# Performance work log

Hardware: AMD Instinct MI355X
Metric: run time of the kernel (lower is better)

Reference implementation:

```python
import jax, jax.numpy as jnp
import numpy as np

G = 512          # graphs per batch
NPG = 90         # nodes per graph (AAL-90 atlas)
N = G * NPG      # 46080 total nodes
DEG = 20
E = N * DEG      # 921600 edges
F_IN = 90
H = 64           # hidden_channels (args.hc)
K = 70           # sort-pool k


def setup_inputs() -> dict:
    key = jax.random.key(0)
    ks = jax.random.split(key, 14)
    x = jax.random.normal(ks[0], (N, F_IN), dtype=jnp.float32)
    # edges kept within each graph (realistic PyG batching)
    gid = jax.random.randint(ks[1], (E,), 0, G)
    src = gid * NPG + jax.random.randint(ks[2], (E,), 0, NPG)
    dst = gid * NPG + jax.random.randint(ks[3], (E,), 0, NPG)
    edge_index = jnp.stack([src, dst]).astype(jnp.int64)
    batch = (jnp.arange(N) // NPG).astype(jnp.int64)
    s_in = 1.0 / np.sqrt(F_IN)
    s_h = 1.0 / np.sqrt(H)
    s_p = 1.0 / np.sqrt(H * K)
    # SAGEConv: out = mean_aggr(x_j) @ W_l + x_i @ W_r + b
    W1l = jax.random.uniform(ks[4], (F_IN, H), jnp.float32, -s_in, s_in)
    W1r = jax.random.uniform(ks[5], (F_IN, H), jnp.float32, -s_in, s_in)
    b1 = jnp.zeros((H,), jnp.float32)
    W2l = jax.random.uniform(ks[6], (H, H), jnp.float32, -s_h, s_h)
    W2r = jax.random.uniform(ks[7], (H, H), jnp.float32, -s_h, s_h)
    b2 = jnp.zeros((H,), jnp.float32)
    Wl1 = jax.random.uniform(ks[8], (H * K, H), jnp.float32, -s_p, s_p)
    bl1 = jax.random.uniform(ks[9], (H,), jnp.float32, -s_p, s_p)
    Wl2 = jax.random.uniform(ks[10], (H, 1), jnp.float32, -s_h, s_h)
    bl2 = jax.random.uniform(ks[11], (1,), jnp.float32, -s_h, s_h)
    return {"x": x, "edge_index": edge_index, "batch": batch,
            "W1l": W1l, "W1r": W1r, "b1": b1,
            "W2l": W2l, "W2r": W2r, "b2": b2,
            "Wl1": Wl1, "bl1": bl1, "Wl2": Wl2, "bl2": bl2}


def sage_conv(x, src, dst, Wl, Wr, b):
    # gather source features, scatter-mean to destinations
    msg = x[src]                                              # [E, F]
    s = jax.ops.segment_sum(msg, dst, num_segments=N)         # [N, F]
    cnt = jax.ops.segment_sum(jnp.ones((src.shape[0], 1), x.dtype),
                              dst, num_segments=N)            # [N, 1]
    mean = s / jnp.maximum(cnt, 1.0)
    return mean @ Wl + x @ Wr + b


def global_sort_pool(x, k):
    # nodes per graph are contiguous and fixed (NPG >= k, no padding needed)
    xr = x.reshape(G, NPG, H)
    order = jnp.argsort(-xr[:, :, -1], axis=1)[:, :k]          # sort by last channel, desc
    top = jnp.take_along_axis(xr, order[:, :, None], axis=1)   # [G, k, H]
    return top.reshape(G, k * H)


def reference(x, edge_index, batch, W1l, W1r, b1, W2l, W2r, b2, Wl1, bl1, Wl2, bl2):
    src, dst = edge_index[0], edge_index[1]
    h = sage_conv(x, src, dst, W1l, W1r, b1)       # conv1
    x_train = h
    h = jax.nn.relu(h)
    h = sage_conv(h, src, dst, W2l, W2r, b2)       # conv2
    p = global_sort_pool(h, K)                     # [G, K*H]
    # dropout is identity at eval time
    p = p @ Wl1 + bl1
    p = p @ Wl2 + bl2
    out = jnp.squeeze(jax.nn.sigmoid(p))           # [G]
    return out, x_train
```

## Files before the change

### kernel.cpp

```cpp
#include <hip/hip_runtime.h>

typedef unsigned short u16;
typedef unsigned int u32;
typedef unsigned char u8;
typedef unsigned long long u64;

#define GG   512
#define NPG  90
#define NTOT (GG*NPG)
#define NED  921600
#define FIN  90
#define HC   64
#define KP   70

#define SAD  90
#define SP   68
#define SR   67
#define SXW  46

#define WF_W1L 0
#define WF_W1R 5760
#define WF_W2L 11520
#define WF_W2R 15616
#define WF_B1  19712
#define WF_B2  19776
#define WF_FOLD 19840
#define WF_ZC  24320
#define WF_FLAG 24321

__device__ __forceinline__ float bf2f(u16 u) {
    union { u32 i; float f; } v; v.i = ((u32)u) << 16; return v.f;
}
__device__ __forceinline__ float bflo(u32 u) {
    union { u32 i; float f; } v; v.i = u << 16; return v.f;
}
__device__ __forceinline__ float bfhi(u32 u) {
    union { u32 i; float f; } v; v.i = u & 0xFFFF0000u; return v.f;
}
__device__ __forceinline__ u16 f2bf(float f) {
    union { float f; u32 i; } v; v.f = f;
    u32 r = (v.i + 0x7FFFu + ((v.i >> 16) & 1u)) >> 16;
    return (u16)r;
}
__device__ __forceinline__ float ldadp(const void* p, long long i, int isf32) {
    return isf32 ? ((const float*)p)[i] : bf2f(((const u16*)p)[i]);
}

__global__ __launch_bounds__(256) void k_pre(
    const u32* __restrict__ xw, const int* __restrict__ ei,
    const void* W1l, const void* W1r, const void* b1,
    const void* W2l, const void* W2r, const void* b2,
    const void* Wl1, const void* bl1, const void* Wl2, const void* bl2,
    float* __restrict__ A, float* __restrict__ wf)
{
    __shared__ int sf;
    const int t = threadIdx.x;
    const int b = blockIdx.x;

    if (b < 900) {
        int lane = t & 63;
        u32 v = (lane < 16) ? (u32)ei[lane] : 0u;
        u64 bb = __ballot((lane & 1) && (v != 0));
        bool wide = (bb == 0ull);
        int e0 = b * 1024 + t * 4;
        int s[4], d[4];
        if (wide) {
            uint4 s01 = *(const uint4*)(ei + 2 * e0);
            uint4 s23 = *(const uint4*)(ei + 2 * e0 + 4);
            uint4 d01 = *(const uint4*)(ei + 2 * (NED + e0));
            uint4 d23 = *(const uint4*)(ei + 2 * (NED + e0) + 4);
            s[0] = (int)s01.x; s[1] = (int)s01.z; s[2] = (int)s23.x; s[3] = (int)s23.z;
            d[0] = (int)d01.x; d[1] = (int)d01.z; d[2] = (int)d23.x; d[3] = (int)d23.z;
        } else {
            uint4 ss = *(const uint4*)(ei + e0);
            uint4 dd = *(const uint4*)(ei + NED + e0);
            s[0] = (int)ss.x; s[1] = (int)ss.y; s[2] = (int)ss.z; s[3] = (int)ss.w;
            d[0] = (int)dd.x; d[1] = (int)dd.y; d[2] = (int)dd.z; d[3] = (int)dd.w;
        }
        #pragma unroll
        for (int k = 0; k < 4; ++k) {
            int dk = d[k];
            if ((unsigned)dk >= NTOT) continue;
            int g = (unsigned)dk / NPG;
            int dl = dk - g * NPG;
            int ls = s[k] - g * NPG;
            if ((unsigned)ls >= NPG) continue;
            atomicAdd(&A[(size_t)g * 8100 + dl * NPG + ls], 1.0f);
        }
        return;
    }

    if (t < 64) {
        u32 e = (xw[t] >> 7) & 0xFF;
        u64 bb = __ballot(e >= 136);
        if (t == 0) sf = (bb != 0ull) ? 1 : 0;
    }
    __syncthreads();
    const int f32 = sf;

    if (b < 978) {
        int i = (b - 900) * 256 + t;
        if      (i < 5760)  wf[i] = ldadp(W1l, i, f32);
        else if (i < 11520) wf[i] = ldadp(W1r, i - 5760, f32);
        else if (i < 15616) wf[i] = ldadp(W2l, i - 11520, f32);
        else if (i < 19712) wf[i] = ldadp(W2r, i - 15616, f32);
        else if (i < 19776) wf[i] = ldadp(b1, i - 19712, f32);
        else if (i < 19840) wf[i] = ldadp(b2, i - 19776, f32);
        if (b == 900 && t == 0) wf[WF_FLAG] = f32 ? 1.0f : 0.0f;
    } else {
        int m = (b - 978) * 256 + t;
        if (m < 4480) {
            float s = 0.f;
            for (int j = 0; j < HC; ++j)
                s += ldadp(Wl1, (long long)m * HC + j, f32) * ldadp(Wl2, j, f32);
            wf[WF_FOLD + m] = s;
        } else if (m == 4480) {
            float s = ldadp(bl2, 0, f32);
            for (int j = 0; j < HC; ++j)
                s += ldadp(bl1, j, f32) * ldadp(Wl2, j, f32);
            wf[WF_ZC] = s;
        }
    }
}

__global__ __launch_bounds__(256, 2) void k_fused(
    const void* __restrict__ x, const float* __restrict__ A,
    const float* __restrict__ wf, void* __restrict__ dout)
{
    __shared__ __align__(16) char smem[57840];
    float* R1   = (float*)smem;
    float* As   = (float*)(smem + 24480);
    float* s_rc = (float*)(smem + 56880);
    float* s_key= (float*)(smem + 57264);
    float* s_red= (float*)(smem + 57648);
    u16*  s_ord = (u16*)(smem + 57680);

    const int g = blockIdx.x;
    const int t = threadIdx.x;
    const bool isf32 = (wf[WF_FLAG] > 0.5f);
    const float* Ag = A + (size_t)g * 8100;
    const float* xg32 = (const float*)x + (size_t)g * 8100;

    for (int p = t; p < 8100; p += 256) As[p] = Ag[p];
    if (!isf32) {
        const u32* src = (const u32*)((const u16*)x + (size_t)g * 8100);
        u32* sxw = (u32*)R1;
        for (int p = t; p < 4050; p += 256) {
            int row = p / 45, c = p - row * 45;
            sxw[row * SXW + c] = src[p];
        }
    }
    __syncthreads();
    if (t < NPG) {
        float s = 0.f;
        for (int k = 0; k < NPG; ++k) s += As[t * SAD + k];
        s_rc[t] = 1.0f / fmaxf(s, 1.0f);
    }

    const int trio = t & 31, jg = t >> 5, jb = jg * 8;
    const int n0 = trio * 3;
    int rows[3];
    #pragma unroll
    for (int i = 0; i < 3; ++i) rows[i] = (n0 + i < NPG) ? n0 + i : 0;

    float accP[3][8], accQ[3][8];
    {
        float4 q0 = *(const float4*)(wf + WF_B1 + jb);
        float4 q1 = *(const float4*)(wf + WF_B1 + jb + 4);
        float bias[8] = {q0.x,q0.y,q0.z,q0.w,q1.x,q1.y,q1.z,q1.w};
        #pragma unroll
        for (int i = 0; i < 3; ++i)
            #pragma unroll
            for (int j = 0; j < 8; ++j) { accP[i][j] = 0.f; accQ[i][j] = bias[j]; }
    }
    {
        const u32* sxw = (const u32*)R1;
        for (int kk = 0; kk < 45; ++kk) {
            const int k0 = 2 * kk;
            const float* wl = wf + WF_W1L + k0 * HC + jb;
            const float* wr = wf + WF_W1R + k0 * HC + jb;
            float4 l00 = *(const float4*)(wl);
            float4 l01 = *(const float4*)(wl + 4);
            float4 l10 = *(const float4*)(wl + HC);
            float4 l11 = *(const float4*)(wl + HC + 4);
            float4 r00 = *(const float4*)(wr);
            float4 r01 = *(const float4*)(wr + 4);
            float4 r10 = *(const float4*)(wr + HC);
            float4 r11 = *(const float4*)(wr + HC + 4);
            float wl0[8] = {l00.x,l00.y,l00.z,l00.w,l01.x,l01.y,l01.z,l01.w};
            float wl1[8] = {l10.x,l10.y,l10.z,l10.w,l11.x,l11.y,l11.z,l11.w};
            float wr0[8] = {r00.x,r00.y,r00.z,r00.w,r01.x,r01.y,r01.z,r01.w};
            float wr1[8] = {r10.x,r10.y,r10.z,r10.w,r11.x,r11.y,r11.z,r11.w};
            float x0[3], x1[3];
            if (!isf32) {
                #pragma unroll
                for (int i = 0; i < 3; ++i) {
                    u32 xv = sxw[rows[i] * SXW + kk];
                    x0[i] = bflo(xv); x1[i] = bfhi(xv);
                }
            } else {
                #pragma unroll
                for (int i = 0; i < 3; ++i) {
                    x0[i] = xg32[rows[i] * FIN + k0];
                    x1[i] = xg32[rows[i] * FIN + k0 + 1];
                }
            }
            #pragma unroll
            for (int i = 0; i < 3; ++i)
                #pragma unroll
                for (int j = 0; j < 8; ++j) {
                    accP[i][j] += x0[i] * wl0[j] + x1[i] * wl1[j];
                    accQ[i][j] += x0[i] * wr0[j] + x1[i] * wr1[j];
                }
        }
    }
    __syncthreads();
    #pragma unroll
    for (int i = 0; i < 3; ++i) {
        int n = n0 + i;
        if (n < NPG) {
            *(float4*)(R1 + n * SP + jb) =
                make_float4(accP[i][0], accP[i][1], accP[i][2], accP[i][3]);
            *(float4*)(R1 + n * SP + jb + 4) =
                make_float4(accP[i][4], accP[i][5], accP[i][6], accP[i][7]);
        }
    }
    __syncthreads();

    float r1v[3][8];
    {
        float accA[3][8];
        #pragma unroll
        for (int i = 0; i < 3; ++i)
            #pragma unroll
            for (int j = 0; j < 8; ++j) accA[i][j] = 0.f;
        for (int k = 0; k < NPG; ++k) {
            float4 p0 = *(const float4*)(R1 + k * SP + jb);
            float4 p1 = *(const float4*)(R1 + k * SP + jb + 4);
            float pv[8] = {p0.x,p0.y,p0.z,p0.w,p1.x,p1.y,p1.z,p1.w};
            float av[3];
            #pragma unroll
            for (int i = 0; i < 3; ++i) av[i] = As[rows[i] * SAD + k];
            #pragma unroll
            for (int i = 0; i < 3; ++i)
                #pragma unroll
                for (int j = 0; j < 8; ++j) accA[i][j] += av[i] * pv[j];
        }
        #pragma unroll
        for (int i = 0; i < 3; ++i) {
            int n = n0 + i;
            if (n < NPG) {
                float rc = s_rc[n];
                float h[8];
                #pragma unroll
                for (int j = 0; j < 8; ++j) h[j] = fmaf(rc, accA[i][j], accQ[i][j]);
                size_t base = 512 + (size_t)(g * NPG + n) * HC + jb;
                if (isf32) {
                    *(float4*)((float*)dout + base) = make_float4(h[0],h[1],h[2],h[3]);
                    *(float4*)((float*)dout + base + 4) = make_float4(h[4],h[5],h[6],h[7]);
                } else {
                    uint4 pk;
                    pk.x = (u32)f2bf(h[0]) | ((u32)f2bf(h[1]) << 16);
                    pk.y = (u32)f2bf(h[2]) | ((u32)f2bf(h[3]) << 16);
                    pk.z = (u32)f2bf(h[4]) | ((u32)f2bf(h[5]) << 16);
                    pk.w = (u32)f2bf(h[6]) | ((u32)f2bf(h[7]) << 16);
                    *(uint4*)((u16*)dout + base) = pk;
                }
                #pragma unroll
                for (int j = 0; j < 8; ++j) r1v[i][j] = fmaxf(h[j], 0.f);
            }
        }
    }
    __syncthreads();
    #pragma unroll
    for (int i = 0; i < 3; ++i) {
        int n = n0 + i;
        if (n < NPG)
            #pragma unroll
            for (int j = 0; j < 8; ++j) R1[n * SR + jb + j] = r1v[i][j];
    }
    __syncthreads();

    {
        float4 q0 = *(const float4*)(wf + WF_B2 + jb);
        float4 q1 = *(const float4*)(wf + WF_B2 + jb + 4);
        float bias[8] = {q0.x,q0.y,q0.z,q0.w,q1.x,q1.y,q1.z,q1.w};
        #pragma unroll
        for (int i = 0; i < 3; ++i)
            #pragma unroll
            for (int j = 0; j < 8; ++j) { accP[i][j] = 0.f; accQ[i][j] = bias[j]; }
    }
    for (int k = 0; k < HC; ++k) {
        const float* wl = wf + WF_W2L + k * HC + jb;
        const float* wr = wf + WF_W2R + k * HC + jb;
        float4 l0 = *(const float4*)(wl);
        float4 l1 = *(const float4*)(wl + 4);
        float4 r0 = *(const float4*)(wr);
        float4 r1q = *(const float4*)(wr + 4);
        float wlv[8] = {l0.x,l0.y,l0.z,l0.w,l1.x,l1.y,l1.z,l1.w};
        float wrv[8] = {r0.x,r0.y,r0.z,r0.w,r1q.x,r1q.y,r1q.z,r1q.w};
        float rv[3];
        #pragma unroll
        for (int i = 0; i < 3; ++i) rv[i] = R1[rows[i] * SR + k];
        #pragma unroll
        for (int i = 0; i < 3; ++i)
            #pragma unroll
            for (int j = 0; j < 8; ++j) {
                accP[i][j] += rv[i] * wlv[j];
                accQ[i][j] += rv[i] * wrv[j];
            }
    }
    __syncthreads();
    #pragma unroll
    for (int i = 0; i < 3; ++i) {
        int n = n0 + i;
        if (n < NPG) {
            *(float4*)(R1 + n * SP + jb) =
                make_float4(accP[i][0], accP[i][1], accP[i][2], accP[i][3]);
            *(float4*)(R1 + n * SP + jb + 4) =
                make_float4(accP[i][4], accP[i][5], accP[i][6], accP[i][7]);
        }
    }
    __syncthreads();

    float h2v[3][8];
    {
        float accA[3][8];
        #pragma unroll
        for (int i = 0; i < 3; ++i)
            #pragma unroll
            for (int j = 0; j < 8; ++j) accA[i][j] = 0.f;
        for (int k = 0; k < NPG; ++k) {
            float4 p0 = *(const float4*)(R1 + k * SP + jb);
            float4 p1 = *(const float4*)(R1 + k * SP + jb + 4);
            float pv[8] = {p0.x,p0.y,p0.z,p0.w,p1.x,p1.y,p1.z,p1.w};
            float av[3];
            #pragma unroll
            for (int i = 0; i < 3; ++i) av[i] = As[rows[i] * SAD + k];
            #pragma unroll
            for (int i = 0; i < 3; ++i)
                #pragma unroll
                for (int j = 0; j < 8; ++j) accA[i][j] += av[i] * pv[j];
        }
        #pragma unroll
        for (int i = 0; i < 3; ++i) {
            int n = n0 + i;
            if (n < NPG) {
                float rc = s_rc[n];
                #pragma unroll
                for (int j = 0; j < 8; ++j)
                    h2v[i][j] = fmaf(rc, accA[i][j], accQ[i][j]);
                if (jg == 7) s_key[n] = h2v[i][7];
            }
        }
    }
    __syncthreads();
    #pragma unroll
    for (int i = 0; i < 3; ++i) {
        int n = n0 + i;
        if (n < NPG)
            #pragma unroll
            for (int j = 0; j < 8; ++j) R1[n * SR + jb + j] = h2v[i][j];
    }
    if (t < NPG) {
        float my = s_key[t];
        int r = 0;
        for (int m2 = 0; m2 < NPG; ++m2) {
            float km = s_key[m2];
            r += (km > my) || (km == my && m2 < t);
        }
        if (r < KP) s_ord[r] = (u16)t;
    }
    __syncthreads();

    float zp = 0.f;
    for (int p = t; p < KP * HC; p += 256) {
        int i = p >> 6, c = p & 63;
        int nn = s_ord[i];
        zp += R1[nn * SR + c] * wf[WF_FOLD + p];
    }
    #pragma unroll
    for (int off = 32; off > 0; off >>= 1) zp += __shfl_down(zp, off);
    if ((t & 63) == 0) s_red[t >> 6] = zp;
    __syncthreads();
    if (t == 0) {
        float z = s_red[0] + s_red[1] + s_red[2] + s_red[3] + wf[WF_ZC];
        float sg = 1.0f / (1.0f + expf(-z));
        if (isf32) ((float*)dout)[g] = sg;
        else       ((u16*)dout)[g]   = f2bf(sg);
    }
}

extern "C" void kernel_launch(void* const* d_in, const int* in_sizes, int n_in,
                              void* d_out, int out_size, void* d_ws, size_t ws_size,
                              hipStream_t stream) {
    const void* x   = d_in[0];
    const int*  ei  = (const int*)d_in[1];
    const void* W1l = d_in[3];
    const void* W1r = d_in[4];
    const void* b1  = d_in[5];
    const void* W2l = d_in[6];
    const void* W2r = d_in[7];
    const void* b2  = d_in[8];
    const void* Wl1 = d_in[9];
    const void* bl1 = d_in[10];
    const void* Wl2 = d_in[11];
    const void* bl2 = d_in[12];

    char* ws   = (char*)d_ws;
    float* A   = (float*)(ws + 64);
    float* wf  = (float*)(ws + 64 + 16588800);

    hipMemsetAsync(A, 0, (size_t)GG * 8100 * sizeof(float), stream);
    k_pre<<<996, 256, 0, stream>>>((const u32*)x, ei, W1l, W1r, b1, W2l, W2r, b2,
                                   Wl1, bl1, Wl2, bl2, A, wf);
    k_fused<<<GG, 256, 0, stream>>>(x, A, wf, d_out);
}
```

Measured before the change: 222.9 us.

## Double fused-kernel block to 512 threads with 4 channels per thread and padded LDS

The fused per-graph kernel now uses 512 threads per block, each owning 3 nodes × 4 channels instead of 3 × 8, which halves per-thread register accumulators and raises wave count per graph. The adjacency and bf16 x tiles in LDS get row padding (91 and 47) to reduce bank conflicts on the strided column reads. The final reduction sums 8 wave partials. This adds more redundant weight and LDS loads per FMA, and with only 512 blocks it may still leave CUs underfilled.

```diff
diff --git a/kernel.cpp b/kernel.cpp
--- a/kernel.cpp
+++ b/kernel.cpp
@@ -13,10 +13,10 @@
 #define HC   64
 #define KP   70
 
-#define SAD  90
+#define SAD  91
 #define SP   68
 #define SR   67
-#define SXW  46
+#define SXW  47
 
 #define WF_W1L 0
 #define WF_W1R 5760
@@ -123,17 +123,17 @@
     }
 }
 
-__global__ __launch_bounds__(256, 2) void k_fused(
+__global__ __launch_bounds__(512, 4) void k_fused(
     const void* __restrict__ x, const float* __restrict__ A,
     const float* __restrict__ wf, void* __restrict__ dout)
 {
-    __shared__ __align__(16) char smem[57840];
+    __shared__ __align__(16) char smem[58176];
     float* R1   = (float*)smem;
     float* As   = (float*)(smem + 24480);
-    float* s_rc = (float*)(smem + 56880);
-    float* s_key= (float*)(smem + 57264);
-    float* s_red= (float*)(smem + 57648);
-    u16*  s_ord = (u16*)(smem + 57680);
+    float* s_rc = (float*)(smem + 57240);
+    float* s_key= (float*)(smem + 57600);
+    float* s_red= (float*)(smem + 57960);
+    u16*  s_ord = (u16*)(smem + 57992);
 
     const int g = blockIdx.x;
     const int t = threadIdx.x;
@@ -141,13 +141,22 @@
     const float* Ag = A + (size_t)g * 8100;
     const float* xg32 = (const float*)x + (size_t)g * 8100;
 
-    for (int p = t; p < 8100; p += 256) As[p] = Ag[p];
+    const int trio = t & 31, sl = t >> 5, jb = sl * 4;
+    const int n0 = trio * 3;
+    int rows[3];
+    #pragma unroll
+    for (int i = 0; i < 3; ++i) rows[i] = (n0 + i < NPG) ? n0 + i : 0;
+
+    for (int p = t; p < 8100; p += 512) {
+        int r = p / NPG, c = p - r * NPG;
+        As[r * SAD + c] = Ag[p];
+    }
     if (!isf32) {
         const u32* src = (const u32*)((const u16*)x + (size_t)g * 8100);
         u32* sxw = (u32*)R1;
-        for (int p = t; p < 4050; p += 256) {
-            int row = p / 45, c = p - row * 45;
-            sxw[row * SXW + c] = src[p];
+        for (int p = t; p < 4050; p += 512) {
+            int r = p / 45, c = p - r * 45;
+            sxw[r * SXW + c] = src[p];
         }
     }
     __syncthreads();
@@ -157,40 +166,27 @@
         s_rc[t] = 1.0f / fmaxf(s, 1.0f);
     }
 
-    const int trio = t & 31, jg = t >> 5, jb = jg * 8;
-    const int n0 = trio * 3;
-    int rows[3];
-    #pragma unroll
-    for (int i = 0; i < 3; ++i) rows[i] = (n0 + i < NPG) ? n0 + i : 0;
-
-    float accP[3][8], accQ[3][8];
-    {
-        float4 q0 = *(const float4*)(wf + WF_B1 + jb);
-        float4 q1 = *(const float4*)(wf + WF_B1 + jb + 4);
-        float bias[8] = {q0.x,q0.y,q0.z,q0.w,q1.x,q1.y,q1.z,q1.w};
+    float accP[3][4], accQ[3][4];
+    {
+        float4 bq = *(const float4*)(wf + WF_B1 + jb);
+        float bias[4] = {bq.x, bq.y, bq.z, bq.w};
         #pragma unroll
         for (int i = 0; i < 3; ++i)
             #pragma unroll
-            for (int j = 0; j < 8; ++j) { accP[i][j] = 0.f; accQ[i][j] = bias[j]; }
+            for (int j = 0; j < 4; ++j) { accP[i][j] = 0.f; accQ[i][j] = bias[j]; }
     }
     {
         const u32* sxw = (const u32*)R1;
         for (int kk = 0; kk < 45; ++kk) {
             const int k0 = 2 * kk;
-            const float* wl = wf + WF_W1L + k0 * HC + jb;
-            const float* wr = wf + WF_W1R + k0 * HC + jb;
-            float4 l00 = *(const float4*)(wl);
-            float4 l01 = *(const float4*)(wl + 4);
-            float4 l10 = *(const float4*)(wl + HC);
-            float4 l11 = *(const float4*)(wl + HC + 4);
-            float4 r00 = *(const float4*)(wr);
-            float4 r01 = *(const float4*)(wr + 4);
-            float4 r10 = *(const float4*)(wr + HC);
-            float4 r11 = *(const float4*)(wr + HC + 4);
-            float wl0[8] = {l00.x,l00.y,l00.z,l00.w,l01.x,l01.y,l01.z,l01.w};
-            float wl1[8] = {l10.x,l10.y,l10.z,l10.w,l11.x,l11.y,l11.z,l11.w};
-            float wr0[8] = {r00.x,r00.y,r00.z,r00.w,r01.x,r01.y,r01.z,r01.w};
-            float wr1[8] = {r10.x,r10.y,r10.z,r10.w,r11.x,r11.y,r11.z,r11.w};
+            float4 l0 = *(const float4*)(wf + WF_W1L + k0 * HC + jb);
+            float4 l1 = *(const float4*)(wf + WF_W1L + (k0 + 1) * HC + jb);
+            float4 r0 = *(const float4*)(wf + WF_W1R + k0 * HC + jb);
+            float4 r1 = *(const float4*)(wf + WF_W1R + (k0 + 1) * HC + jb);
+            float wl0[4] = {l0.x,l0.y,l0.z,l0.w};
+            float wl1[4] = {l1.x,l1.y,l1.z,l1.w};
+            float wr0[4] = {r0.x,r0.y,r0.z,r0.w};
+            float wr1[4] = {r1.x,r1.y,r1.z,r1.w};
             float x0[3], x1[3];
             if (!isf32) {
                 #pragma unroll
@@ -208,7 +204,7 @@
             #pragma unroll
             for (int i = 0; i < 3; ++i)
                 #pragma unroll
-                for (int j = 0; j < 8; ++j) {
+                for (int j = 0; j < 4; ++j) {
                     accP[i][j] += x0[i] * wl0[j] + x1[i] * wl1[j];
                     accQ[i][j] += x0[i] * wr0[j] + x1[i] * wr1[j];
                 }
@@ -218,56 +214,49 @@
     #pragma unroll
     for (int i = 0; i < 3; ++i) {
         int n = n0 + i;
-        if (n < NPG) {
+        if (n < NPG)
             *(float4*)(R1 + n * SP + jb) =
                 make_float4(accP[i][0], accP[i][1], accP[i][2], accP[i][3]);
-            *(float4*)(R1 + n * SP + jb + 4) =
-                make_float4(accP[i][4], accP[i][5], accP[i][6], accP[i][7]);
-        }
-    }
-    __syncthreads();
-
-    float r1v[3][8];
-    {
-        float accA[3][8];
+    }
+    __syncthreads();
+
+    float r1v[3][4];
+    {
+        float accA[3][4];
         #pragma unroll
         for (int i = 0; i < 3; ++i)
             #pragma unroll
-            for (int j = 0; j < 8; ++j) accA[i][j] = 0.f;
+            for (int j = 0; j < 4; ++j) accA[i][j] = 0.f;
         for (int k = 0; k < NPG; ++k) {
-            float4 p0 = *(const float4*)(R1 + k * SP + jb);
-            float4 p1 = *(const float4*)(R1 + k * SP + jb + 4);
-            float pv[8] = {p0.x,p0.y,p0.z,p0.w,p1.x,p1.y,p1.z,p1.w};
+            float4 pv4 = *(const float4*)(R1 + k * SP + jb);
+            float pv[4] = {pv4.x, pv4.y, pv4.z, pv4.w};
             float av[3];
             #pragma unroll
             for (int i = 0; i < 3; ++i) av[i] = As[rows[i] * SAD + k];
             #pragma unroll
             for (int i = 0; i < 3; ++i)
                 #pragma unroll
-                for (int j = 0; j < 8; ++j) accA[i][j] += av[i] * pv[j];
+                for (int j = 0; j < 4; ++j) accA[i][j] += av[i] * pv[j];
         }
         #pragma unroll
         for (int i = 0; i < 3; ++i) {
             int n = n0 + i;
             if (n < NPG) {
                 float rc = s_rc[n];
-                float h[8];
-                #pragma unroll
-                for (int j = 0; j < 8; ++j) h[j] = fmaf(rc, accA[i][j], accQ[i][j]);
+                float h[4];
+                #pragma unroll
+                for (int j = 0; j < 4; ++j) h[j] = fmaf(rc, accA[i][j], accQ[i][j]);
                 size_t base = 512 + (size_t)(g * NPG + n) * HC + jb;
                 if (isf32) {
                     *(float4*)((float*)dout + base) = make_float4(h[0],h[1],h[2],h[3]);
-                    *(float4*)((float*)dout + base + 4) = make_float4(h[4],h[5],h[6],h[7]);
                 } else {
-                    uint4 pk;
+                    uint2 pk;
                     pk.x = (u32)f2bf(h[0]) | ((u32)f2bf(h[1]) << 16);
                     pk.y = (u32)f2bf(h[2]) | ((u32)f2bf(h[3]) << 16);
-                    pk.z = (u32)f2bf(h[4]) | ((u32)f2bf(h[5]) << 16);
-                    pk.w = (u32)f2bf(h[6]) | ((u32)f2bf(h[7]) << 16);
-                    *(uint4*)((u16*)dout + base) = pk;
+                    *(uint2*)((u16*)dout + base) = pk;
                 }
                 #pragma unroll
-                for (int j = 0; j < 8; ++j) r1v[i][j] = fmaxf(h[j], 0.f);
+                for (int j = 0; j < 4; ++j) r1v[i][j] = fmaxf(h[j], 0.f);
             }
         }
     }
@@ -277,70 +266,65 @@
         int n = n0 + i;
         if (n < NPG)
             #pragma unroll
-            for (int j = 0; j < 8; ++j) R1[n * SR + jb + j] = r1v[i][j];
-    }
-    __syncthreads();
-
-    {
-        float4 q0 = *(const float4*)(wf + WF_B2 + jb);
-        float4 q1 = *(const float4*)(wf + WF_B2 + jb + 4);
-        float bias[8] = {q0.x,q0.y,q0.z,q0.w,q1.x,q1.y,q1.z,q1.w};
+            for (int j = 0; j < 4; ++j) R1[n * SR + jb + j] = r1v[i][j];
+    }
+    __syncthreads();
+
+    {
+        float4 bq = *(const float4*)(wf + WF_B2 + jb);
+        float bias[4] = {bq.x, bq.y, bq.z, bq.w};
         #pragma unroll
         for (int i = 0; i < 3; ++i)
             #pragma unroll
-            for (int j = 0; j < 8; ++j) { accP[i][j] = 0.f; accQ[i][j] = bias[j]; }
-    }
-    for (int k = 0; k < HC; ++k) {
-        const float* wl = wf + WF_W2L + k * HC + jb;
-        const float* wr = wf + WF_W2R + k * HC + jb;
-        float4 l0 = *(const float4*)(wl);
-        float4 l1 = *(const float4*)(wl + 4);
-        float4 r0 = *(const float4*)(wr);
-        float4 r1q = *(const float4*)(wr + 4);
-        float wlv[8] = {l0.x,l0.y,l0.z,l0.w,l1.x,l1.y,l1.z,l1.w};
-        float wrv[8] = {r0.x,r0.y,r0.z,r0.w,r1q.x,r1q.y,r1q.z,r1q.w};
-        float rv[3];
-        #pragma unroll
-        for (int i = 0; i < 3; ++i) rv[i] = R1[rows[i] * SR + k];
-        #pragma unroll
-        for (int i = 0; i < 3; ++i)
-            #pragma unroll
-            for (int j = 0; j < 8; ++j) {
-                accP[i][j] += rv[i] * wlv[j];
-                accQ[i][j] += rv[i] * wrv[j];
+            for (int j = 0; j < 4; ++j) { accP[i][j] = 0.f; accQ[i][j] = bias[j]; }
+    }
+    {
+        int rws[3];
+        #pragma unroll
+        for (int i = 0; i < 3; ++i) rws[i] = rows[i] * SR;
+        for (int k = 0; k < HC; ++k) {
+            float4 l = *(const float4*)(wf + WF_W2L + k * HC + jb);
+            float4 r = *(const float4*)(wf + WF_W2R + k * HC + jb);
+            float wlv[4] = {l.x,l.y,l.z,l.w};
+            float wrv[4] = {r.x,r.y,r.z,r.w};
+            #pragma unroll
+            for (int i = 0; i < 3; ++i) {
+                float rv = R1[rws[i] + k];
+                #pragma unroll
+                for (int j = 0; j < 4; ++j) {
+                    accP[i][j] += rv * wlv[j];
+                    accQ[i][j] += rv * wrv[j];
+                }
             }
+        }
     }
     __syncthreads();
     #pragma unroll
     for (int i = 0; i < 3; ++i) {
         int n = n0 + i;
-        if (n < NPG) {
+        if (n < NPG)
             *(float4*)(R1 + n * SP + jb) =
                 make_float4(accP[i][0], accP[i][1], accP[i][2], accP[i][3]);
-            *(float4*)(R1 + n * SP + jb + 4) =
-                make_float4(accP[i][4], accP[i][5], accP[i][6], accP[i][7]);
-        }
-    }
-    __syncthreads();
-
-    float h2v[3][8];
-    {
-        float accA[3][8];
+    }
+    __syncthreads();
+
+    float h2v[3][4];
+    {
+        float accA[3][4];
         #pragma unroll
         for (int i = 0; i < 3; ++i)
             #pragma unroll
-            for (int j = 0; j < 8; ++j) accA[i][j] = 0.f;
+            for (int j = 0; j < 4; ++j) accA[i][j] = 0.f;
         for (int k = 0; k < NPG; ++k) {
-            float4 p0 = *(const float4*)(R1 + k * SP + jb);
-            float4 p1 = *(const float4*)(R1 + k * SP + jb + 4);
-            float pv[8] = {p0.x,p0.y,p0.z,p0.w,p1.x,p1.y,p1.z,p1.w};
+            float4 pv4 = *(const float4*)(R1 + k * SP + jb);
+            float pv[4] = {pv4.x, pv4.y, pv4.z, pv4.w};
             float av[3];
             #pragma unroll
             for (int i = 0; i < 3; ++i) av[i] = As[rows[i] * SAD + k];
             #pragma unroll
             for (int i = 0; i < 3; ++i)
                 #pragma unroll
-                for (int j = 0; j < 8; ++j) accA[i][j] += av[i] * pv[j];
+                for (int j = 0; j < 4; ++j) accA[i][j] += av[i] * pv[j];
         }
         #pragma unroll
         for (int i = 0; i < 3; ++i) {
@@ -348,9 +332,9 @@
             if (n < NPG) {
                 float rc = s_rc[n];
                 #pragma unroll
-                for (int j = 0; j < 8; ++j)
+                for (int j = 0; j < 4; ++j)
                     h2v[i][j] = fmaf(rc, accA[i][j], accQ[i][j]);
-                if (jg == 7) s_key[n] = h2v[i][7];
+                if (sl == 15) s_key[n] = h2v[i][3];
             }
         }
     }
@@ -360,7 +344,7 @@
         int n = n0 + i;
         if (n < NPG)
             #pragma unroll
-            for (int j = 0; j < 8; ++j) R1[n * SR + jb + j] = h2v[i][j];
+            for (int j = 0; j < 4; ++j) R1[n * SR + jb + j] = h2v[i][j];
     }
     if (t < NPG) {
         float my = s_key[t];
@@ -374,7 +358,7 @@
     __syncthreads();
 
     float zp = 0.f;
-    for (int p = t; p < KP * HC; p += 256) {
+    for (int p = t; p < KP * HC; p += 512) {
         int i = p >> 6, c = p & 63;
         int nn = s_ord[i];
         zp += R1[nn * SR + c] * wf[WF_FOLD + p];
@@ -384,7 +368,9 @@
     if ((t & 63) == 0) s_red[t >> 6] = zp;
     __syncthreads();
     if (t == 0) {
-        float z = s_red[0] + s_red[1] + s_red[2] + s_red[3] + wf[WF_ZC];
+        float z = wf[WF_ZC];
+        #pragma unroll
+        for (int i = 0; i < 8; ++i) z += s_red[i];
         float sg = 1.0f / (1.0f + expf(-z));
         if (isf32) ((float*)dout)[g] = sg;
         else       ((u16*)dout)[g]   = f2bf(sg);
@@ -414,5 +400,5 @@
     hipMemsetAsync(A, 0, (size_t)GG * 8100 * sizeof(float), stream);
     k_pre<<<996, 256, 0, stream>>>((const u32*)x, ei, W1l, W1r, b1, W2l, W2r, b2,
                                    Wl1, bl1, Wl2, bl2, A, wf);
-    k_fused<<<GG, 256, 0, stream>>>(x, A, wf, d_out);
-}
+    k_fused<<<GG, 512, 0, stream>>>(x, A, wf, d_out);
+}
```

After: 233.8 us. 4.9% more time.
